# Optimization experiments

Hardware: AMD Instinct MI355X
Metric: run time of the kernel (lower is better)

## Reference

```python
import jax, jax.numpy as jnp
import numpy as np

N, T, IN, H, OUT, E = 50000, 12, 2, 128, 12, 800000


def setup_inputs() -> dict:
    key = jax.random.key(0)
    ks = jax.random.split(key, 20)
    s_in = 1.0 / np.sqrt(H)

    def w(k, shape):
        return jax.random.uniform(k, shape, jnp.float32, -s_in, s_in)

    return {
        "x": jax.random.normal(ks[0], (N, T, IN), jnp.float32),
        "edge_index": jax.random.randint(ks[1], (2, E), 0, N, dtype=jnp.int32),
        # LSTM layer 0 (input_dim -> H), gate order i,f,g,o as in PyTorch
        "Wih0": w(ks[2], (4 * H, IN)), "Whh0": w(ks[3], (4 * H, H)),
        "bih0": w(ks[4], (4 * H,)), "bhh0": w(ks[5], (4 * H,)),
        # LSTM layer 1 (H -> H)
        "Wih1": w(ks[6], (4 * H, H)), "Whh1": w(ks[7], (4 * H, H)),
        "bih1": w(ks[8], (4 * H,)), "bhh1": w(ks[9], (4 * H,)),
        # GCN layers
        "W0": w(ks[10], (H, H)), "b0": w(ks[11], (H,)),
        "W1": w(ks[12], (H, H)), "b1": w(ks[13], (H,)),
        "W2": w(ks[14], (H, OUT)), "b2": w(ks[15], (OUT,)),
    }


def _lstm_layer(seq, Wih, Whh, bih, bhh):
    # seq: [T, N, D] -> outputs [T, N, H]
    n = seq.shape[1]
    h0 = jnp.zeros((n, H), seq.dtype)
    c0 = jnp.zeros((n, H), seq.dtype)
    b = bih + bhh

    def step(carry, xt):
        h, c = carry
        z = xt @ Wih.T + h @ Whh.T + b
        i, f, g, o = jnp.split(z, 4, axis=-1)
        c = jax.nn.sigmoid(f) * c + jax.nn.sigmoid(i) * jnp.tanh(g)
        h = jax.nn.sigmoid(o) * jnp.tanh(c)
        return (h, c), h

    _, ys = jax.lax.scan(step, (h0, c0), seq)
    return ys


def _gcn(h, W, b, src, dst, norm):
    # x @ W, gather sources, edge-normalize, scatter-add to targets, + bias
    hW = h @ W
    msg = hW[src] * norm[:, None]
    return jax.ops.segment_sum(msg, dst, num_segments=N) + b


def reference(x, edge_index, Wih0, Whh0, bih0, bhh0, Wih1, Whh1, bih1, bhh1,
              W0, b0, W1, b1, W2, b2):
    # 2-layer LSTM over node time series (dropout inactive at inference)
    seq = jnp.transpose(x, (1, 0, 2))          # [T, N, IN]
    y0 = _lstm_layer(seq, Wih0, Whh0, bih0, bhh0)
    y1 = _lstm_layer(y0, Wih1, Whh1, bih1, bhh1)
    h = y1[-1]                                  # last timestep: [N, H]

    # GCN normalization with self-loops (symmetric, all edge weights 1)
    loops = jnp.arange(N, dtype=edge_index.dtype)
    src = jnp.concatenate([edge_index[0], loops])
    dst = jnp.concatenate([edge_index[1], loops])
    deg = jax.ops.segment_sum(jnp.ones(src.shape[0], h.dtype), dst, num_segments=N)
    dinv = jax.lax.rsqrt(deg)                   # deg >= 1 thanks to self-loops
    norm = dinv[src] * dinv[dst]

    h = jax.nn.relu(_gcn(h, W0, b0, src, dst, norm))
    h = jax.nn.relu(_gcn(h, W1, b1, src, dst, norm))
    out = _gcn(h, W2, b2, src, dst, norm)       # [N, OUT]
    return out
```

## Files before the change

kernel.cpp:

```cpp
#include <hip/hip_runtime.h>
#include <hip/hip_bf16.h>

#define TT 12
#define HDIM 128
#define ODIM 12
#define KS0 136
#define TPAD 36

typedef short bf16x8 __attribute__((ext_vector_type(8)));
typedef float f32x16 __attribute__((ext_vector_type(16)));
typedef float f32x4  __attribute__((ext_vector_type(4)));

__device__ __forceinline__ float fastrcp(float x) { return __builtin_amdgcn_rcpf(x); }
__device__ __forceinline__ float sigf(float x) { return fastrcp(1.f + __expf(-x)); }
__device__ __forceinline__ float tanh_fast(float x) { return 1.f - 2.f * fastrcp(1.f + __expf(2.f * x)); }
__device__ __forceinline__ unsigned short f2bf(float f) {
    union { float f; unsigned int u; } v; v.f = f;
    unsigned int r = v.u + 0x7FFFu + ((v.u >> 16) & 1u);
    return (unsigned short)(r >> 16);
}

__global__ void pack_kernel(const float* __restrict__ Whh0, const float* __restrict__ Wih1,
                            const float* __restrict__ Whh1, unsigned short* __restrict__ Wpk)
{
    int idx = blockIdx.x * 256 + threadIdx.x;
    if (idx >= 384 * 64) return;
    int lane = idx & 63;
    int slot = idx >> 6;
    int mat = slot >> 7;
    int rem = slot & 127;
    if (mat == 0) {
        int cb = rem >> 3, s = rem & 7;
        int col = cb * 32 + (lane & 31);
#pragma unroll
        for (int j = 0; j < 8; ++j) {
            int k = s * 16 + ((lane >> 5) << 3) + j;
            Wpk[((size_t)(slot * 64 + lane) << 3) + j] = f2bf(Whh0[col * 128 + k]);
        }
    } else {
        const float* src = (mat == 1) ? Wih1 : Whh1;
        int ct = rem >> 2, ks = rem & 3;
        int col = ct * 16 + (lane & 15);
#pragma unroll
        for (int j = 0; j < 8; ++j) {
            int k = ks * 32 + ((lane >> 4) << 3) + j;
            Wpk[((size_t)(slot * 64 + lane) << 3) + j] = f2bf(src[col * 128 + k]);
        }
    }
}

__global__ __launch_bounds__(512, 1) void lstm_l0_kernel(
    const float* __restrict__ x,
    const unsigned short* __restrict__ Wpk,
    const float* __restrict__ Wih0,
    const float* __restrict__ bih0, const float* __restrict__ bhh0,
    unsigned short* __restrict__ h0f,
    int N, int ntiles)
{
    __shared__ unsigned short wlds[65536];
    __shared__ unsigned short hA0[64 * KS0];
    __shared__ float xls[64 * 24];

    const int tid  = threadIdx.x;
    const int w    = tid >> 6;
    const int ln   = tid & 63;
    const int ln31 = ln & 31;
    const int half = ln >> 5;
    const int wsub = w & 3;
    const int rb   = w >> 2;
    const int col  = wsub * 32 + ln31;

    for (int i = tid * 8; i < 65536; i += 512 * 8)
        *(bf16x8*)(wlds + i) = *(const bf16x8*)(Wpk + i);

    float wx0[4], wx1[4], br0[4];
#pragma unroll
    for (int g = 0; g < 4; ++g) {
        int row = (g << 7) + col;
        wx0[g] = Wih0[row * 2 + 0];
        wx1[g] = Wih0[row * 2 + 1];
        br0[g] = bih0[row] + bhh0[row];
    }

    for (int tile = blockIdx.x; tile < ntiles; tile += gridDim.x) {
        const int nbase = tile * 64;
        __syncthreads();
        for (int i = tid; i < 64 * 24; i += 512) {
            int n = nbase + i / 24;
            xls[i] = (n < N) ? x[nbase * 24 + i] : 0.f;
        }
        for (int i = tid; i < 64 * KS0; i += 512) hA0[i] = 0;
        float c0[16];
#pragma unroll
        for (int r = 0; r < 16; ++r) c0[r] = 0.f;
        __syncthreads();

        for (int t = 0; t < TT; ++t) {
            f32x16 acc[4];
#pragma unroll
            for (int g = 0; g < 4; ++g)
#pragma unroll
                for (int e = 0; e < 16; ++e) acc[g][e] = 0.f;
#pragma unroll
            for (int s = 0; s < 8; ++s) {
                bf16x8 a = *(const bf16x8*)(hA0 + (rb * 32 + ln31) * KS0 + s * 16 + half * 8);
#pragma unroll
                for (int g = 0; g < 4; ++g) {
                    int cb = g * 4 + wsub;
                    bf16x8 b = *(const bf16x8*)(wlds + (((cb * 8 + s) * 64 + ln) << 3));
                    acc[g] = __builtin_amdgcn_mfma_f32_32x32x16_bf16(a, b, acc[g], 0, 0, 0);
                }
            }
            __syncthreads();
#pragma unroll
            for (int r = 0; r < 16; ++r) {
                int node = rb * 32 + (r & 3) + 8 * (r >> 2) + 4 * half;
                float xa = xls[node * 24 + t * 2 + 0];
                float xb = xls[node * 24 + t * 2 + 1];
                float zi = acc[0][r] + br0[0] + wx0[0] * xa + wx1[0] * xb;
                float zf = acc[1][r] + br0[1] + wx0[1] * xa + wx1[1] * xb;
                float zg = acc[2][r] + br0[2] + wx0[2] * xa + wx1[2] * xb;
                float zo = acc[3][r] + br0[3] + wx0[3] * xa + wx1[3] * xb;
                float cn = sigf(zf) * c0[r] + sigf(zi) * tanh_fast(zg);
                c0[r] = cn;
                float h = sigf(zo) * tanh_fast(cn);
                hA0[node * KS0 + col] = f2bf(h);
            }
            __syncthreads();
            {
                unsigned short* dt = h0f + (((size_t)(tile * TT + t)) << 13);
#pragma unroll
                for (int it = 0; it < 2; ++it) {
                    int i = tid + it * 512;
                    int rtks = i >> 6;
                    int lane = i & 63;
                    int m   = ((rtks >> 2) << 4) + (lane & 15);
                    int chb = ((rtks & 3) << 5) + ((lane >> 4) << 3);
                    bf16x8 v = *(const bf16x8*)(hA0 + m * KS0 + chb);
                    *(bf16x8*)(dt + ((size_t)i << 3)) = v;
                }
            }
        }
    }
}

__global__ __launch_bounds__(512) void lstm_l1f_kernel(
    const unsigned short* __restrict__ h0f,
    const unsigned short* __restrict__ Wpk,
    const float* __restrict__ bih1, const float* __restrict__ bhh1,
    float* __restrict__ hbuf,
    int N, int ntiles)
{
    __shared__ unsigned short wlds[65536];
    __shared__ unsigned short hA1[2][8192];

    const int tid  = threadIdx.x;
    const int w    = tid >> 6;
    const int ln   = tid & 63;
    const int l15  = ln & 15;
    const int quad = ln >> 4;
    const int ch   = w * 16 + l15;
    const int chk  = ch >> 5;
    const int chq  = (ch >> 3) & 3;
    const int chj  = ch & 7;

    for (int i = tid * 8; i < 65536; i += 512 * 8)
        *(bf16x8*)(wlds + i) = *(const bf16x8*)(Wpk + 131072 + i);

    bf16x8 wfr[4][4];
#pragma unroll
    for (int g = 0; g < 4; ++g)
#pragma unroll
        for (int ks = 0; ks < 4; ++ks) {
            int slot = (g * 8 + w) * 4 + ks;
            wfr[g][ks] = *(const bf16x8*)(Wpk + 65536 + ((size_t)(slot * 64 + ln) << 3));
        }

    float br1[4];
#pragma unroll
    for (int g = 0; g < 4; ++g) {
        int row = (g << 7) + ch;
        br1[g] = bih1[row] + bhh1[row];
    }

    const bf16x8 zv = {0, 0, 0, 0, 0, 0, 0, 0};
    __syncthreads();

    for (int tile = blockIdx.x; tile < ntiles; tile += gridDim.x) {
        __syncthreads();
        for (int i = tid; i < 1024; i += 512)
            *(bf16x8*)(hA1[0] + i * 8) = zv;
        float c1[16];
#pragma unroll
        for (int r = 0; r < 16; ++r) c1[r] = 0.f;
        __syncthreads();

        for (int t = 0; t < TT; ++t) {
            const unsigned short* usp = hA1[t & 1];
            unsigned short* dst = hA1[(t & 1) ^ 1];
            const unsigned short* h0t = h0f + (((size_t)(tile * TT + t)) << 13);

            f32x4 acc[4][4];
#pragma unroll
            for (int rt = 0; rt < 4; ++rt)
#pragma unroll
                for (int g = 0; g < 4; ++g)
#pragma unroll
                    for (int e = 0; e < 4; ++e) acc[rt][g][e] = 0.f;

#pragma unroll
            for (int ks = 0; ks < 4; ++ks) {
                bf16x8 a0[4];
#pragma unroll
                for (int rt = 0; rt < 4; ++rt)
                    a0[rt] = *(const bf16x8*)(h0t + (((rt * 4 + ks) * 64 + ln) << 3));
                bf16x8 a1[4];
#pragma unroll
                for (int rt = 0; rt < 4; ++rt)
                    a1[rt] = *(const bf16x8*)(usp + (((rt * 4 + ks) * 64 + ln) << 3));
#pragma unroll
                for (int g = 0; g < 4; ++g) {
                    int slot = (g * 8 + w) * 4 + ks;
                    bf16x8 b = *(const bf16x8*)(wlds + ((size_t)(slot * 64 + ln) << 3));
#pragma unroll
                    for (int rt = 0; rt < 4; ++rt)
                        acc[rt][g] = __builtin_amdgcn_mfma_f32_16x16x32_bf16(a1[rt], b, acc[rt][g], 0, 0, 0);
                }
#pragma unroll
                for (int g = 0; g < 4; ++g)
#pragma unroll
                    for (int rt = 0; rt < 4; ++rt)
                        acc[rt][g] = __builtin_amdgcn_mfma_f32_16x16x32_bf16(a0[rt], wfr[g][ks], acc[rt][g], 0, 0, 0);
            }

#pragma unroll
            for (int rt = 0; rt < 4; ++rt) {
#pragma unroll
                for (int rg = 0; rg < 4; ++rg) {
                    int ci = rt * 4 + rg;
                    float zi = acc[rt][0][rg] + br1[0];
                    float zf = acc[rt][1][rg] + br1[1];
                    float zg = acc[rt][2][rg] + br1[2];
                    float zo = acc[rt][3][rg] + br1[3];
                    float cn = sigf(zf) * c1[ci] + sigf(zi) * tanh_fast(zg);
                    c1[ci] = cn;
                    float h = sigf(zo) * tanh_fast(cn);
                    if (t + 1 < TT) {
                        dst[(((rt * 4 + chk) * 64 + chq * 16 + quad * 4 + rg) << 3) + chj] = f2bf(h);
                    } else {
                        int n = tile * 64 + rt * 16 + quad * 4 + rg;
                        if (n < N) hbuf[n * HDIM + ch] = h;
                    }
                }
            }
            __syncthreads();
        }
    }
}

__global__ void deg_count_kernel(const int* __restrict__ ei, int* __restrict__ degi, int E)
{
    int e = blockIdx.x * 256 + threadIdx.x;
    if (e < E) atomicAdd(&degi[ei[E + e]], 1);
}

__global__ void row_alloc_kernel(const int* __restrict__ degi, int* __restrict__ row_ptr,
                                 float* __restrict__ dinv, int* __restrict__ counter, int N)
{
    int n = blockIdx.x * 256 + threadIdx.x;
    int lane = threadIdx.x & 63;
    int v = (n < N) ? degi[n] : 0;
    int incl = v;
    for (int off = 1; off < 64; off <<= 1) {
        int u = __shfl_up(incl, off);
        if (lane >= off) incl += u;
    }
    int base = 0;
    if (lane == 63) base = atomicAdd(counter, incl);
    base = __shfl(base, 63);
    if (n < N) {
        row_ptr[n] = base + (incl - v);
        dinv[n] = rsqrtf((float)(v + 1));
    }
}

__global__ void csr_fill_kernel(const int* __restrict__ ei, const int* __restrict__ row_ptr,
                                int* __restrict__ fill, int* __restrict__ csr_src, int E)
{
    int e = blockIdx.x * 256 + threadIdx.x;
    if (e < E) {
        int d = ei[E + e];
        int p = atomicAdd(&fill[d], 1);
        csr_src[row_ptr[d] + p] = ei[e];
    }
}

__global__ __launch_bounds__(256) void gemm128_kernel(const float* __restrict__ X,
                                                      const float* __restrict__ W,
                                                      _Float16* __restrict__ Y, int N)
{
    __shared__ float XT[128 * TPAD];
    const int tid = threadIdx.x;
    const int nbase = blockIdx.x * 32;
    for (int idx = tid; idx < 32 * 128; idx += 256) {
        int m = idx >> 7, k = idx & 127;
        int n = nbase + m;
        XT[k * TPAD + m] = (n < N) ? X[n * HDIM + k] : 0.f;
    }
    __syncthreads();
    const int c  = tid & 63;
    const int mb = (tid >> 6) << 3;
    float acc[8][2];
#pragma unroll
    for (int i = 0; i < 8; ++i) { acc[i][0] = 0.f; acc[i][1] = 0.f; }
    for (int k = 0; k < 128; ++k) {
        const float* xr = &XT[k * TPAD + mb];
        float4 a0 = *(const float4*)(xr);
        float4 a1 = *(const float4*)(xr + 4);
        float a[8] = {a0.x, a0.y, a0.z, a0.w, a1.x, a1.y, a1.z, a1.w};
        float b0 = W[k * HDIM + c];
        float b1 = W[k * HDIM + c + 64];
#pragma unroll
        for (int i = 0; i < 8; ++i) {
            acc[i][0] = fmaf(a[i], b0, acc[i][0]);
            acc[i][1] = fmaf(a[i], b1, acc[i][1]);
        }
    }
#pragma unroll
    for (int i = 0; i < 8; ++i) {
        int n = nbase + mb + i;
        if (n < N) {
            Y[n * HDIM + c]      = (_Float16)acc[i][0];
            Y[n * HDIM + c + 64] = (_Float16)acc[i][1];
        }
    }
}

__global__ void gemm12_kernel(const float* __restrict__ X, const float* __restrict__ W2,
                              _Float16* __restrict__ Y, int N)
{
    int idx = blockIdx.x * 256 + threadIdx.x;
    int n = idx / ODIM, c = idx - n * ODIM;
    if (n >= N) return;
    float acc = 0.f;
    for (int k = 0; k < 128; ++k) acc = fmaf(X[n * HDIM + k], W2[k * ODIM + c], acc);
    Y[n * ODIM + c] = (_Float16)acc;
}

__global__ __launch_bounds__(128) void agg128_kernel(const _Float16* __restrict__ hW,
        const int* __restrict__ row_ptr, const int* __restrict__ degi,
        const int* __restrict__ csr_src, const float* __restrict__ dinv,
        const float* __restrict__ bias, float* __restrict__ out, int N, int do_relu)
{
    int n = blockIdx.x;
    int c = threadIdx.x;
    float dn = dinv[n];
    float acc = (float)hW[n * HDIM + c] * dn * dn;
    int start = row_ptr[n];
    int cnt = degi[n];
    for (int i = 0; i < cnt; ++i) {
        int s = csr_src[start + i];
        acc = fmaf((float)hW[s * HDIM + c], dinv[s] * dn, acc);
    }
    float v = acc + bias[c];
    if (do_relu) v = fmaxf(v, 0.f);
    out[n * HDIM + c] = v;
}

__global__ void agg12_kernel(const _Float16* __restrict__ hW, const int* __restrict__ row_ptr,
        const int* __restrict__ degi, const int* __restrict__ csr_src,
        const float* __restrict__ dinv, const float* __restrict__ b2,
        float* __restrict__ out, int N)
{
    int idx = blockIdx.x * 256 + threadIdx.x;
    int n = idx / ODIM, c = idx - n * ODIM;
    if (n >= N) return;
    float dn = dinv[n];
    float acc = (float)hW[n * ODIM + c] * dn * dn;
    int start = row_ptr[n], cnt = degi[n];
    for (int i = 0; i < cnt; ++i) {
        int s = csr_src[start + i];
        acc = fmaf((float)hW[s * ODIM + c], dinv[s] * dn, acc);
    }
    out[n * ODIM + c] = acc + b2[c];
}

extern "C" void kernel_launch(void* const* d_in, const int* in_sizes, int n_in,
                              void* d_out, int out_size, void* d_ws, size_t ws_size,
                              hipStream_t stream)
{
    const float* x     = (const float*)d_in[0];
    const int*   ei    = (const int*)d_in[1];
    const float* Wih0  = (const float*)d_in[2];
    const float* Whh0  = (const float*)d_in[3];
    const float* bih0  = (const float*)d_in[4];
    const float* bhh0  = (const float*)d_in[5];
    const float* Wih1  = (const float*)d_in[6];
    const float* Whh1  = (const float*)d_in[7];
    const float* bih1  = (const float*)d_in[8];
    const float* bhh1  = (const float*)d_in[9];
    const float* W0    = (const float*)d_in[10];
    const float* b0    = (const float*)d_in[11];
    const float* W1    = (const float*)d_in[12];
    const float* b1    = (const float*)d_in[13];
    const float* W2    = (const float*)d_in[14];
    const float* b2    = (const float*)d_in[15];
    float* out = (float*)d_out;

    const int N = in_sizes[0] / (TT * 2);
    const int E = in_sizes[1] / 2;
    const int ntiles = (N + 63) / 64;

    unsigned short* Wpk = (unsigned short*)d_ws;
    float* fbase = (float*)((char*)d_ws + 393216);
    float* hbuf = fbase;
    float* buf1 = hbuf + (size_t)N * HDIM;
    float* buf2 = buf1 + (size_t)N * HDIM;
    float* dinv = buf2 + (size_t)N * HDIM;
    int* degi    = (int*)(dinv + N);
    int* fill    = degi + N;
    int* counter = fill + N;
    int* row_ptr = counter + 1;
    int* csr_src = row_ptr + N;
    size_t h0_off = (((size_t)((char*)(csr_src + E) - (char*)d_ws)) + 255) & ~(size_t)255;
    unsigned short* h0f = (unsigned short*)((char*)d_ws + h0_off);
    _Float16* buf1h = (_Float16*)buf1;

    hipMemsetAsync(degi, 0, (size_t)(2 * N + 1) * sizeof(int), stream);

    pack_kernel<<<(384 * 64 + 255) / 256, 256, 0, stream>>>(Whh0, Wih1, Whh1, Wpk);

    lstm_l0_kernel<<<256, 512, 0, stream>>>(x, Wpk, Wih0, bih0, bhh0, h0f, N, ntiles);
    lstm_l1f_kernel<<<256, 512, 0, stream>>>(h0f, Wpk, bih1, bhh1, hbuf, N, ntiles);

    deg_count_kernel<<<(E + 255) / 256, 256, 0, stream>>>(ei, degi, E);
    row_alloc_kernel<<<(N + 255) / 256, 256, 0, stream>>>(degi, row_ptr, dinv, counter, N);
    csr_fill_kernel<<<(E + 255) / 256, 256, 0, stream>>>(ei, row_ptr, fill, csr_src, E);

    gemm128_kernel<<<(N + 31) / 32, 256, 0, stream>>>(hbuf, W0, buf1h, N);
    agg128_kernel<<<N, 128, 0, stream>>>(buf1h, row_ptr, degi, csr_src, dinv, b0, buf2, N, 1);
    gemm128_kernel<<<(N + 31) / 32, 256, 0, stream>>>(buf2, W1, buf1h, N);
    agg128_kernel<<<N, 128, 0, stream>>>(buf1h, row_ptr, degi, csr_src, dinv, b1, buf2, N, 1);
    gemm12_kernel<<<((size_t)N * ODIM + 255) / 256, 256, 0, stream>>>(buf2, W2, buf1h, N);
    agg12_kernel<<<((size_t)N * ODIM + 255) / 256, 256, 0, stream>>>(
        buf1h, row_ptr, degi, csr_src, dinv, b2, out, N);
}
```

Before: 940.2 us.

## Keep LSTM weights in registers, one tile per block, unroll aggregation loops

Both LSTM kernels now keep their recurrent and input weight fragments in registers instead of a 128 KB LDS copy. They launch one block per 64-node tile instead of looping over tiles in a persistent grid, and launch bounds allow two blocks per CU. Layer 0 switches to the 16x16x32 MFMA layout with double-buffered h and writes h0 one step late to overlap the stores. The GCN aggregation kernels handle two nodes per block and unroll the neighbor loop four times with independent accumulators for more memory-level parallelism. Holding the weights in registers raises register pressure and may cause spills at two blocks per CU.

```diff
diff --git a/kernel.cpp b/kernel.cpp
--- a/kernel.cpp
+++ b/kernel.cpp
@@ -4,11 +4,9 @@
 #define TT 12
 #define HDIM 128
 #define ODIM 12
-#define KS0 136
 #define TPAD 36
 
 typedef short bf16x8 __attribute__((ext_vector_type(8)));
-typedef float f32x16 __attribute__((ext_vector_type(16)));
 typedef float f32x4  __attribute__((ext_vector_type(4)));
 
 __device__ __forceinline__ float fastrcp(float x) { return __builtin_amdgcn_rcpf(x); }
@@ -29,130 +27,26 @@
     int slot = idx >> 6;
     int mat = slot >> 7;
     int rem = slot & 127;
-    if (mat == 0) {
-        int cb = rem >> 3, s = rem & 7;
-        int col = cb * 32 + (lane & 31);
-#pragma unroll
-        for (int j = 0; j < 8; ++j) {
-            int k = s * 16 + ((lane >> 5) << 3) + j;
-            Wpk[((size_t)(slot * 64 + lane) << 3) + j] = f2bf(Whh0[col * 128 + k]);
-        }
-    } else {
-        const float* src = (mat == 1) ? Wih1 : Whh1;
-        int ct = rem >> 2, ks = rem & 3;
-        int col = ct * 16 + (lane & 15);
-#pragma unroll
-        for (int j = 0; j < 8; ++j) {
-            int k = ks * 32 + ((lane >> 4) << 3) + j;
-            Wpk[((size_t)(slot * 64 + lane) << 3) + j] = f2bf(src[col * 128 + k]);
-        }
-    }
-}
-
-__global__ __launch_bounds__(512, 1) void lstm_l0_kernel(
+    const float* src = (mat == 0) ? Whh0 : (mat == 1) ? Wih1 : Whh1;
+    int ct = rem >> 2, ks = rem & 3;
+    int col = ct * 16 + (lane & 15);
+#pragma unroll
+    for (int j = 0; j < 8; ++j) {
+        int k = ks * 32 + ((lane >> 4) << 3) + j;
+        Wpk[((size_t)(slot * 64 + lane) << 3) + j] = f2bf(src[col * 128 + k]);
+    }
+}
+
+__global__ __launch_bounds__(512, 2) void lstm_l0_kernel(
     const float* __restrict__ x,
     const unsigned short* __restrict__ Wpk,
     const float* __restrict__ Wih0,
     const float* __restrict__ bih0, const float* __restrict__ bhh0,
     unsigned short* __restrict__ h0f,
-    int N, int ntiles)
-{
-    __shared__ unsigned short wlds[65536];
-    __shared__ unsigned short hA0[64 * KS0];
+    int N)
+{
+    __shared__ unsigned short hA0[2][8192];
     __shared__ float xls[64 * 24];
-
-    const int tid  = threadIdx.x;
-    const int w    = tid >> 6;
-    const int ln   = tid & 63;
-    const int ln31 = ln & 31;
-    const int half = ln >> 5;
-    const int wsub = w & 3;
-    const int rb   = w >> 2;
-    const int col  = wsub * 32 + ln31;
-
-    for (int i = tid * 8; i < 65536; i += 512 * 8)
-        *(bf16x8*)(wlds + i) = *(const bf16x8*)(Wpk + i);
-
-    float wx0[4], wx1[4], br0[4];
-#pragma unroll
-    for (int g = 0; g < 4; ++g) {
-        int row = (g << 7) + col;
-        wx0[g] = Wih0[row * 2 + 0];
-        wx1[g] = Wih0[row * 2 + 1];
-        br0[g] = bih0[row] + bhh0[row];
-    }
-
-    for (int tile = blockIdx.x; tile < ntiles; tile += gridDim.x) {
-        const int nbase = tile * 64;
-        __syncthreads();
-        for (int i = tid; i < 64 * 24; i += 512) {
-            int n = nbase + i / 24;
-            xls[i] = (n < N) ? x[nbase * 24 + i] : 0.f;
-        }
-        for (int i = tid; i < 64 * KS0; i += 512) hA0[i] = 0;
-        float c0[16];
-#pragma unroll
-        for (int r = 0; r < 16; ++r) c0[r] = 0.f;
-        __syncthreads();
-
-        for (int t = 0; t < TT; ++t) {
-            f32x16 acc[4];
-#pragma unroll
-            for (int g = 0; g < 4; ++g)
-#pragma unroll
-                for (int e = 0; e < 16; ++e) acc[g][e] = 0.f;
-#pragma unroll
-            for (int s = 0; s < 8; ++s) {
-                bf16x8 a = *(const bf16x8*)(hA0 + (rb * 32 + ln31) * KS0 + s * 16 + half * 8);
-#pragma unroll
-                for (int g = 0; g < 4; ++g) {
-                    int cb = g * 4 + wsub;
-                    bf16x8 b = *(const bf16x8*)(wlds + (((cb * 8 + s) * 64 + ln) << 3));
-                    acc[g] = __builtin_amdgcn_mfma_f32_32x32x16_bf16(a, b, acc[g], 0, 0, 0);
-                }
-            }
-            __syncthreads();
-#pragma unroll
-            for (int r = 0; r < 16; ++r) {
-                int node = rb * 32 + (r & 3) + 8 * (r >> 2) + 4 * half;
-                float xa = xls[node * 24 + t * 2 + 0];
-                float xb = xls[node * 24 + t * 2 + 1];
-                float zi = acc[0][r] + br0[0] + wx0[0] * xa + wx1[0] * xb;
-                float zf = acc[1][r] + br0[1] + wx0[1] * xa + wx1[1] * xb;
-                float zg = acc[2][r] + br0[2] + wx0[2] * xa + wx1[2] * xb;
-                float zo = acc[3][r] + br0[3] + wx0[3] * xa + wx1[3] * xb;
-                float cn = sigf(zf) * c0[r] + sigf(zi) * tanh_fast(zg);
-                c0[r] = cn;
-                float h = sigf(zo) * tanh_fast(cn);
-                hA0[node * KS0 + col] = f2bf(h);
-            }
-            __syncthreads();
-            {
-                unsigned short* dt = h0f + (((size_t)(tile * TT + t)) << 13);
-#pragma unroll
-                for (int it = 0; it < 2; ++it) {
-                    int i = tid + it * 512;
-                    int rtks = i >> 6;
-                    int lane = i & 63;
-                    int m   = ((rtks >> 2) << 4) + (lane & 15);
-                    int chb = ((rtks & 3) << 5) + ((lane >> 4) << 3);
-                    bf16x8 v = *(const bf16x8*)(hA0 + m * KS0 + chb);
-                    *(bf16x8*)(dt + ((size_t)i << 3)) = v;
-                }
-            }
-        }
-    }
-}
-
-__global__ __launch_bounds__(512) void lstm_l1f_kernel(
-    const unsigned short* __restrict__ h0f,
-    const unsigned short* __restrict__ Wpk,
-    const float* __restrict__ bih1, const float* __restrict__ bhh1,
-    float* __restrict__ hbuf,
-    int N, int ntiles)
-{
-    __shared__ unsigned short wlds[65536];
-    __shared__ unsigned short hA1[2][8192];
 
     const int tid  = threadIdx.x;
     const int w    = tid >> 6;
@@ -160,20 +54,131 @@
     const int l15  = ln & 15;
     const int quad = ln >> 4;
     const int ch   = w * 16 + l15;
-    const int chk  = ch >> 5;
-    const int chq  = (ch >> 3) & 3;
-    const int chj  = ch & 7;
-
-    for (int i = tid * 8; i < 65536; i += 512 * 8)
-        *(bf16x8*)(wlds + i) = *(const bf16x8*)(Wpk + 131072 + i);
-
-    bf16x8 wfr[4][4];
+    const int chk  = ch >> 5, chq = (ch >> 3) & 3, chj = ch & 7;
+    const int tile = blockIdx.x;
+    const int nbase = tile * 64;
+
+    bf16x8 whr[4][4];
 #pragma unroll
     for (int g = 0; g < 4; ++g)
 #pragma unroll
         for (int ks = 0; ks < 4; ++ks) {
             int slot = (g * 8 + w) * 4 + ks;
-            wfr[g][ks] = *(const bf16x8*)(Wpk + 65536 + ((size_t)(slot * 64 + ln) << 3));
+            whr[g][ks] = *(const bf16x8*)(Wpk + ((size_t)(slot * 64 + ln) << 3));
+        }
+
+    float wx0[4], wx1[4], br0[4];
+#pragma unroll
+    for (int g = 0; g < 4; ++g) {
+        int row = (g << 7) + ch;
+        wx0[g] = Wih0[row * 2 + 0];
+        wx1[g] = Wih0[row * 2 + 1];
+        br0[g] = bih0[row] + bhh0[row];
+    }
+
+    const bf16x8 zv = {0, 0, 0, 0, 0, 0, 0, 0};
+    for (int i = tid; i < 64 * 24; i += 512) {
+        int n = nbase + i / 24;
+        xls[i] = (n < N) ? x[nbase * 24 + i] : 0.f;
+    }
+    for (int i = tid; i < 1024; i += 512)
+        *(bf16x8*)(hA0[0] + i * 8) = zv;
+    float c0[16];
+#pragma unroll
+    for (int r = 0; r < 16; ++r) c0[r] = 0.f;
+    __syncthreads();
+
+    for (int t = 0; t < TT; ++t) {
+        const unsigned short* usp = hA0[t & 1];
+        unsigned short* dst = hA0[(t & 1) ^ 1];
+
+        f32x4 acc[4][4];
+#pragma unroll
+        for (int rt = 0; rt < 4; ++rt)
+#pragma unroll
+            for (int g = 0; g < 4; ++g)
+#pragma unroll
+                for (int e = 0; e < 4; ++e) acc[rt][g][e] = 0.f;
+
+#pragma unroll
+        for (int ks = 0; ks < 4; ++ks) {
+            bf16x8 a[4];
+#pragma unroll
+            for (int rt = 0; rt < 4; ++rt)
+                a[rt] = *(const bf16x8*)(usp + (((rt * 4 + ks) * 64 + ln) << 3));
+#pragma unroll
+            for (int g = 0; g < 4; ++g)
+#pragma unroll
+                for (int rt = 0; rt < 4; ++rt)
+                    acc[rt][g] = __builtin_amdgcn_mfma_f32_16x16x32_bf16(a[rt], whr[g][ks], acc[rt][g], 0, 0, 0);
+        }
+
+        if (t > 0) {
+            unsigned short* dt = h0f + (((size_t)(tile * TT + (t - 1))) << 13);
+#pragma unroll
+            for (int it = 0; it < 2; ++it) {
+                int i = tid + it * 512;
+                *(bf16x8*)(dt + ((size_t)i << 3)) = *(const bf16x8*)(usp + ((size_t)i << 3));
+            }
+        }
+
+#pragma unroll
+        for (int rt = 0; rt < 4; ++rt) {
+#pragma unroll
+            for (int rg = 0; rg < 4; ++rg) {
+                int ci = rt * 4 + rg;
+                int nd = rt * 16 + quad * 4 + rg;
+                float xa = xls[nd * 24 + t * 2 + 0];
+                float xb = xls[nd * 24 + t * 2 + 1];
+                float zi = acc[rt][0][rg] + br0[0] + wx0[0] * xa + wx1[0] * xb;
+                float zf = acc[rt][1][rg] + br0[1] + wx0[1] * xa + wx1[1] * xb;
+                float zg = acc[rt][2][rg] + br0[2] + wx0[2] * xa + wx1[2] * xb;
+                float zo = acc[rt][3][rg] + br0[3] + wx0[3] * xa + wx1[3] * xb;
+                float cn = sigf(zf) * c0[ci] + sigf(zi) * tanh_fast(zg);
+                c0[ci] = cn;
+                float h = sigf(zo) * tanh_fast(cn);
+                dst[(((rt * 4 + chk) * 64 + chq * 16 + quad * 4 + rg) << 3) + chj] = f2bf(h);
+            }
+        }
+        __syncthreads();
+    }
+    {
+        const unsigned short* usp = hA0[TT & 1];
+        unsigned short* dt = h0f + (((size_t)(tile * TT + (TT - 1))) << 13);
+#pragma unroll
+        for (int it = 0; it < 2; ++it) {
+            int i = tid + it * 512;
+            *(bf16x8*)(dt + ((size_t)i << 3)) = *(const bf16x8*)(usp + ((size_t)i << 3));
+        }
+    }
+}
+
+__global__ __launch_bounds__(512, 2) void lstm_l1f_kernel(
+    const unsigned short* __restrict__ h0f,
+    const unsigned short* __restrict__ Wpk,
+    const float* __restrict__ bih1, const float* __restrict__ bhh1,
+    float* __restrict__ hbuf,
+    int N)
+{
+    __shared__ unsigned short hA1[2][8192];
+
+    const int tid  = threadIdx.x;
+    const int w    = tid >> 6;
+    const int ln   = tid & 63;
+    const int l15  = ln & 15;
+    const int quad = ln >> 4;
+    const int ch   = w * 16 + l15;
+    const int chk  = ch >> 5, chq = (ch >> 3) & 3, chj = ch & 7;
+    const int tile = blockIdx.x;
+
+    bf16x8 wfr[4][4], whr[4][4];
+#pragma unroll
+    for (int g = 0; g < 4; ++g)
+#pragma unroll
+        for (int ks = 0; ks < 4; ++ks) {
+            int slot = (g * 8 + w) * 4 + ks;
+            wfr[g][ks] = *(const bf16x8*)(Wpk + 65536  + ((size_t)(slot * 64 + ln) << 3));
+            whr[g][ks] = *(const bf16x8*)(Wpk + 131072 + ((size_t)(slot * 64 + ln) << 3));
         }
 
     float br1[4];
@@ -184,77 +189,69 @@
     }
 
     const bf16x8 zv = {0, 0, 0, 0, 0, 0, 0, 0};
+    for (int i = tid; i < 1024; i += 512)
+        *(bf16x8*)(hA1[0] + i * 8) = zv;
+    float c1[16];
+#pragma unroll
+    for (int r = 0; r < 16; ++r) c1[r] = 0.f;
     __syncthreads();
 
-    for (int tile = blockIdx.x; tile < ntiles; tile += gridDim.x) {
-        __syncthreads();
-        for (int i = tid; i < 1024; i += 512)
-            *(bf16x8*)(hA1[0] + i * 8) = zv;
-        float c1[16];
-#pragma unroll
-        for (int r = 0; r < 16; ++r) c1[r] = 0.f;
-        __syncthreads();
-
-        for (int t = 0; t < TT; ++t) {
-            const unsigned short* usp = hA1[t & 1];
-            unsigned short* dst = hA1[(t & 1) ^ 1];
-            const unsigned short* h0t = h0f + (((size_t)(tile * TT + t)) << 13);
-
-            f32x4 acc[4][4];
+    for (int t = 0; t < TT; ++t) {
+        const unsigned short* usp = hA1[t & 1];
+        unsigned short* dst = hA1[(t & 1) ^ 1];
+        const unsigned short* h0t = h0f + (((size_t)(tile * TT + t)) << 13);
+
+        f32x4 acc[4][4];
+#pragma unroll
+        for (int rt = 0; rt < 4; ++rt)
+#pragma unroll
+            for (int g = 0; g < 4; ++g)
+#pragma unroll
+                for (int e = 0; e < 4; ++e) acc[rt][g][e] = 0.f;
+
+#pragma unroll
+        for (int ks = 0; ks < 4; ++ks) {
+            bf16x8 a0[4];
 #pragma unroll
             for (int rt = 0; rt < 4; ++rt)
-#pragma unroll
-                for (int g = 0; g < 4; ++g)
-#pragma unroll
-                    for (int e = 0; e < 4; ++e) acc[rt][g][e] = 0.f;
-
-#pragma unroll
-            for (int ks = 0; ks < 4; ++ks) {
-                bf16x8 a0[4];
+                a0[rt] = *(const bf16x8*)(h0t + (((rt * 4 + ks) * 64 + ln) << 3));
+            bf16x8 a1[4];
+#pragma unroll
+            for (int rt = 0; rt < 4; ++rt)
+                a1[rt] = *(const bf16x8*)(usp + (((rt * 4 + ks) * 64 + ln) << 3));
+#pragma unroll
+            for (int g = 0; g < 4; ++g)
 #pragma unroll
                 for (int rt = 0; rt < 4; ++rt)
-                    a0[rt] = *(const bf16x8*)(h0t + (((rt * 4 + ks) * 64 + ln) << 3));
-                bf16x8 a1[4];
+                    acc[rt][g] = __builtin_amdgcn_mfma_f32_16x16x32_bf16(a1[rt], whr[g][ks], acc[rt][g], 0, 0, 0);
+#pragma unroll
+            for (int g = 0; g < 4; ++g)
 #pragma unroll
                 for (int rt = 0; rt < 4; ++rt)
-                    a1[rt] = *(const bf16x8*)(usp + (((rt * 4 + ks) * 64 + ln) << 3));
-#pragma unroll
-                for (int g = 0; g < 4; ++g) {
-                    int slot = (g * 8 + w) * 4 + ks;
-                    bf16x8 b = *(const bf16x8*)(wlds + ((size_t)(slot * 64 + ln) << 3));
-#pragma unroll
-                    for (int rt = 0; rt < 4; ++rt)
-                        acc[rt][g] = __builtin_amdgcn_mfma_f32_16x16x32_bf16(a1[rt], b, acc[rt][g], 0, 0, 0);
-                }
-#pragma unroll
-                for (int g = 0; g < 4; ++g)
-#pragma unroll
-                    for (int rt = 0; rt < 4; ++rt)
-                        acc[rt][g] = __builtin_amdgcn_mfma_f32_16x16x32_bf16(a0[rt], wfr[g][ks], acc[rt][g], 0, 0, 0);
-            }
-
-#pragma unroll
-            for (int rt = 0; rt < 4; ++rt) {
-#pragma unroll
-                for (int rg = 0; rg < 4; ++rg) {
-                    int ci = rt * 4 + rg;
-                    float zi = acc[rt][0][rg] + br1[0];
-                    float zf = acc[rt][1][rg] + br1[1];
-                    float zg = acc[rt][2][rg] + br1[2];
-                    float zo = acc[rt][3][rg] + br1[3];
-                    float cn = sigf(zf) * c1[ci] + sigf(zi) * tanh_fast(zg);
-                    c1[ci] = cn;
-                    float h = sigf(zo) * tanh_fast(cn);
-                    if (t + 1 < TT) {
-                        dst[(((rt * 4 + chk) * 64 + chq * 16 + quad * 4 + rg) << 3) + chj] = f2bf(h);
-                    } else {
-                        int n = tile * 64 + rt * 16 + quad * 4 + rg;
-                        if (n < N) hbuf[n * HDIM + ch] = h;
-                    }
+                    acc[rt][g] = __builtin_amdgcn_mfma_f32_16x16x32_bf16(a0[rt], wfr[g][ks], acc[rt][g], 0, 0, 0);
+        }
+
+#pragma unroll
+        for (int rt = 0; rt < 4; ++rt) {
+#pragma unroll
+            for (int rg = 0; rg < 4; ++rg) {
+                int ci = rt * 4 + rg;
+                float zi = acc[rt][0][rg] + br1[0];
+                float zf = acc[rt][1][rg] + br1[1];
+                float zg = acc[rt][2][rg] + br1[2];
+                float zo = acc[rt][3][rg] + br1[3];
+                float cn = sigf(zf) * c1[ci] + sigf(zi) * tanh_fast(zg);
+                c1[ci] = cn;
+                float h = sigf(zo) * tanh_fast(cn);
+                if (t + 1 < TT) {
+                    dst[(((rt * 4 + chk) * 64 + chq * 16 + quad * 4 + rg) << 3) + chj] = f2bf(h);
+                } else {
+                    int n = tile * 64 + rt * 16 + quad * 4 + rg;
+                    if (n < N) hbuf[n * HDIM + ch] = h;
                 }
             }
-            __syncthreads();
-        }
+        }
+        __syncthreads();
     }
 }
 
@@ -347,22 +344,40 @@
     Y[n * ODIM + c] = (_Float16)acc;
 }
 
-__global__ __launch_bounds__(128) void agg128_kernel(const _Float16* __restrict__ hW,
+__global__ __launch_bounds__(256) void agg128_kernel(const _Float16* __restrict__ hW,
         const int* __restrict__ row_ptr, const int* __restrict__ degi,
         const int* __restrict__ csr_src, const float* __restrict__ dinv,
         const float* __restrict__ bias, float* __restrict__ out, int N, int do_relu)
 {
-    int n = blockIdx.x;
-    int c = threadIdx.x;
+    int n = blockIdx.x * 2 + (threadIdx.x >> 7);
+    int c = threadIdx.x & 127;
+    if (n >= N) return;
     float dn = dinv[n];
-    float acc = (float)hW[n * HDIM + c] * dn * dn;
-    int start = row_ptr[n];
-    int cnt = degi[n];
-    for (int i = 0; i < cnt; ++i) {
+    float a0 = (float)hW[n * HDIM + c] * dn * dn;
+    float a1 = 0.f, a2 = 0.f, a3 = 0.f;
+    int start = row_ptr[n], cnt = degi[n];
+    int i = 0;
+    for (; i + 4 <= cnt; i += 4) {
+        int s0 = csr_src[start + i];
+        int s1 = csr_src[start + i + 1];
+        int s2 = csr_src[start + i + 2];
+        int s3 = csr_src[start + i + 3];
+        float w0 = dinv[s0] * dn, w1 = dinv[s1] * dn;
+        float w2 = dinv[s2] * dn, w3 = dinv[s3] * dn;
+        float v0 = (float)hW[s0 * HDIM + c];
+        float v1 = (float)hW[s1 * HDIM + c];
+        float v2 = (float)hW[s2 * HDIM + c];
+        float v3 = (float)hW[s3 * HDIM + c];
+        a0 = fmaf(v0, w0, a0);
+        a1 = fmaf(v1, w1, a1);
+        a2 = fmaf(v2, w2, a2);
+        a3 = fmaf(v3, w3, a3);
+    }
+    for (; i < cnt; ++i) {
         int s = csr_src[start + i];
-        acc = fmaf((float)hW[s * HDIM + c], dinv[s] * dn, acc);
-    }
-    float v = acc + bias[c];
+        a0 = fmaf((float)hW[s * HDIM + c], dinv[s] * dn, a0);
+    }
+    float v = (a0 + a1) + (a2 + a3) + bias[c];
     if (do_relu) v = fmaxf(v, 0.f);
     out[n * HDIM + c] = v;
 }
@@ -376,13 +391,25 @@
     int n = idx / ODIM, c = idx - n * ODIM;
     if (n >= N) return;
     float dn = dinv[n];
-    float acc = (float)hW[n * ODIM + c] * dn * dn;
+    float a0 = (float)hW[n * ODIM + c] * dn * dn;
+    float a1 = 0.f, a2 = 0.f, a3 = 0.f;
     int start = row_ptr[n], cnt = degi[n];
-    for (int i = 0; i < cnt; ++i) {
+    int i = 0;
+    for (; i + 4 <= cnt; i += 4) {
+        int s0 = csr_src[start + i];
+        int s1 = csr_src[start + i + 1];
+        int s2 = csr_src[start + i + 2];
+        int s3 = csr_src[start + i + 3];
+        a0 = fmaf((float)hW[s0 * ODIM + c], dinv[s0] * dn, a0);
+        a1 = fmaf((float)hW[s1 * ODIM + c], dinv[s1] * dn, a1);
+        a2 = fmaf((float)hW[s2 * ODIM + c], dinv[s2] * dn, a2);
+        a3 = fmaf((float)hW[s3 * ODIM + c], dinv[s3] * dn, a3);
+    }
+    for (; i < cnt; ++i) {
         int s = csr_src[start + i];
-        acc = fmaf((float)hW[s * ODIM + c], dinv[s] * dn, acc);
-    }
-    out[n * ODIM + c] = acc + b2[c];
+        a0 = fmaf((float)hW[s * ODIM + c], dinv[s] * dn, a0);
+    }
+    out[n * ODIM + c] = (a0 + a1) + (a2 + a3) + b2[c];
 }
 
 extern "C" void kernel_launch(void* const* d_in, const int* in_sizes, int n_in,
@@ -430,17 +457,17 @@
 
     pack_kernel<<<(384 * 64 + 255) / 256, 256, 0, stream>>>(Whh0, Wih1, Whh1, Wpk);
 
-    lstm_l0_kernel<<<256, 512, 0, stream>>>(x, Wpk, Wih0, bih0, bhh0, h0f, N, ntiles);
-    lstm_l1f_kernel<<<256, 512, 0, stream>>>(h0f, Wpk, bih1, bhh1, hbuf, N, ntiles);
+    lstm_l0_kernel<<<ntiles, 512, 0, stream>>>(x, Wpk, Wih0, bih0, bhh0, h0f, N);
+    lstm_l1f_kernel<<<ntiles, 512, 0, stream>>>(h0f, Wpk, bih1, bhh1, hbuf, N);
 
     deg_count_kernel<<<(E + 255) / 256, 256, 0, stream>>>(ei, degi, E);
     row_alloc_kernel<<<(N + 255) / 256, 256, 0, stream>>>(degi, row_ptr, dinv, counter, N);
     csr_fill_kernel<<<(E + 255) / 256, 256, 0, stream>>>(ei, row_ptr, fill, csr_src, E);
 
     gemm128_kernel<<<(N + 31) / 32, 256, 0, stream>>>(hbuf, W0, buf1h, N);
-    agg128_kernel<<<N, 128, 0, stream>>>(buf1h, row_ptr, degi, csr_src, dinv, b0, buf2, N, 1);
+    agg128_kernel<<<(N + 1) / 2, 256, 0, stream>>>(buf1h, row_ptr, degi, csr_src, dinv, b0, buf2, N, 1);
     gemm128_kernel<<<(N + 31) / 32, 256, 0, stream>>>(buf2, W1, buf1h, N);
-    agg128_kernel<<<N, 128, 0, stream>>>(buf1h, row_ptr, degi, csr_src, dinv, b1, buf2, N, 1);
+    agg128_kernel<<<(N + 1) / 2, 256, 0, stream>>>(buf1h, row_ptr, degi, csr_src, dinv, b1, buf2, N, 1);
     gemm12_kernel<<<((size_t)N * ODIM + 255) / 256, 256, 0, stream>>>(buf2, W2, buf1h, N);
     agg12_kernel<<<((size_t)N * ODIM + 255) / 256, 256, 0, stream>>>(
         buf1h, row_ptr, degi, csr_src, dinv, b2, out, N);
```

New measurement: 988.4 us. +5.1%, slower.
